# Kernel optimization log

Measured on AMD Instinct MI355X. Metric: run time of the kernel, lower is better.

Reference implementation:

```python
import jax, jax.numpy as jnp
import numpy as np

B, A, L, M, E = 4096, 64, 16, 4, 10
K = (4, 16, 32)
Q = (2, 4, 6)
P = (32, 128, 256)


def setup_inputs() -> dict:
    key = jax.random.key(0)
    ks = iter(jax.random.split(key, 32))
    inp = {}
    inp['x'] = jax.random.normal(next(ks), (B, A, L, M), dtype=jnp.float32)
    inp['y'] = jax.random.uniform(next(ks), (B, E), dtype=jnp.float32)
    inp['w1'] = jax.random.normal(next(ks), (E, K[0], Q[0], A), dtype=jnp.float32) / (K[0] * Q[0])
    inp['w2'] = jax.random.normal(next(ks), (E, K[1], Q[1], A), dtype=jnp.float32) / (K[1] * Q[1])
    inp['w3'] = jax.random.normal(next(ks), (E, K[2], Q[2], A), dtype=jnp.float32) / (K[2] * Q[2])
    inp['coeff1'] = jax.random.normal(next(ks), (P[0],), dtype=jnp.float32)
    inp['coeff2'] = jax.random.normal(next(ks), (P[1],), dtype=jnp.float32)
    inp['coeff3'] = jax.random.normal(next(ks), (P[2],), dtype=jnp.float32)
    ri = lambda n, hi: jax.random.randint(next(ks), (n,), 0, hi, dtype=jnp.int32)
    inp['i1'] = ri(P[0], L); inp['l1'] = ri(P[0], M)
    inp['k1'] = ri(P[0], K[0]); inp['q1'] = ri(P[0], Q[0])
    inp['i2'] = ri(P[1], L); inp['j2'] = ri(P[1], L)
    inp['l2'] = ri(P[1], M); inp['m2'] = ri(P[1], M)
    inp['k2'] = ri(P[1], K[1]); inp['q2'] = ri(P[1], Q[1])
    inp['i3'] = ri(P[2], L); inp['j3'] = ri(P[2], L); inp['f3'] = ri(P[2], L)
    inp['l3'] = ri(P[2], M); inp['m3'] = ri(P[2], M); inp['g3'] = ri(P[2], M)
    inp['k3'] = ri(P[2], K[2]); inp['q3'] = ri(P[2], Q[2])
    return inp


def _forward(x, y, w1, w2, w3, coeff1, coeff2, coeff3,
             i1, l1, k1, q1,
             i2, j2, l2, m2, k2, q2,
             i3, j3, f3, l3, m3, g3, k3, q3):
    # element-mixed weights: [B, K, Q, A]
    wy1 = jnp.einsum('ekqa,be->bkqa', w1, y)
    wy2 = jnp.einsum('ekqa,be->bkqa', w2, y)
    wy3 = jnp.einsum('ekqa,be->bkqa', w3, y)
    # sparse path contraction (equivalent to dense 'ik,lq,ekqa,bail,be->ba' etc.)
    g1 = jnp.transpose(wy1[:, k1, q1, :], (0, 2, 1))          # [B, A, P1]
    t1 = jnp.einsum('bap,p->ba', x[:, :, i1, l1] * g1, coeff1)
    g2 = jnp.transpose(wy2[:, k2, q2, :], (0, 2, 1))          # [B, A, P2]
    t2 = jnp.einsum('bap,p->ba', x[:, :, i2, l2] * x[:, :, j2, m2] * g2, coeff2)
    g3_ = jnp.transpose(wy3[:, k3, q3, :], (0, 2, 1))         # [B, A, P3]
    t3 = jnp.einsum('bap,p->ba',
                    x[:, :, i3, l3] * x[:, :, j3, m3] * x[:, :, f3, g3] * g3_,
                    coeff3)
    return t1 + t2 + t3  # [B, A] (scalar irrep_out -> flattened view)


def reference(x, y, w1, w2, w3, coeff1, coeff2, coeff3,
              i1, l1, k1, q1,
              i2, j2, l2, m2, k2, q2,
              i3, j3, f3, l3, m3, g3, k3, q3):
    return _forward(x, y, w1, w2, w3, coeff1, coeff2, coeff3,
                    i1, l1, k1, q1,
                    i2, j2, l2, m2, k2, q2,
                    i3, j3, f3, l3, m3, g3, k3, q3)
```

## Files before the change

kernel.cpp:

```cpp
#include <hip/hip_runtime.h>
#include <hip/hip_bf16.h>

typedef _Float16 f16x8 __attribute__((ext_vector_type(8)));
typedef _Float16 f16x4 __attribute__((ext_vector_type(4)));
typedef float    f32x4 __attribute__((ext_vector_type(4)));

constexpr int BB  = 4096;
constexpr int AA  = 64;
constexpr int ED  = 10;
constexpr int P1N = 32, P2N = 128, P3N = 256;
constexpr int PT  = 416;
constexpr int NKS = 13;
constexpr int BCH = 64;
constexpr int NCH = 4;

__global__ void build_idx_kernel(
    const int* __restrict__ i1, const int* __restrict__ l1,
    const int* __restrict__ i2, const int* __restrict__ j2,
    const int* __restrict__ l2, const int* __restrict__ m2,
    const int* __restrict__ i3, const int* __restrict__ j3,
    const int* __restrict__ f3, const int* __restrict__ l3,
    const int* __restrict__ m3, const int* __restrict__ g3,
    unsigned* __restrict__ idxs) {
  const int p = threadIdx.x;
  if (p >= PT) return;
  unsigned sa, sb = 64, sc = 64;
  if (p < P1N) {
    sa = i1[p] * 4 + l1[p];
  } else if (p < P1N + P2N) {
    int pp = p - P1N;
    sa = i2[pp] * 4 + l2[pp];
    sb = j2[pp] * 4 + m2[pp];
  } else {
    int pp = p - P1N - P2N;
    sa = i3[pp] * 4 + l3[pp];
    sb = j3[pp] * 4 + m3[pp];
    sc = f3[pp] * 4 + g3[pp];
  }
  idxs[p] = (sa * 8) | ((sb * 8) << 10) | ((sc * 8) << 20);
}

__global__ void build_cwb_kernel(
    const float* __restrict__ w1, const float* __restrict__ w2, const float* __restrict__ w3,
    const float* __restrict__ c1, const float* __restrict__ c2, const float* __restrict__ c3,
    const int* __restrict__ k1, const int* __restrict__ q1,
    const int* __restrict__ k2, const int* __restrict__ q2,
    const int* __restrict__ k3, const int* __restrict__ q3,
    _Float16* __restrict__ cwb) {
  const int a  = blockIdx.x & 63;
  const int ks = blockIdx.x >> 6;
  const int l  = threadIdx.x;
  const int grp = l >> 4, e = l & 15;
  _Float16* dst = cwb + (((size_t)a * NKS + ks) * 64 + l) * 8;
  #pragma unroll
  for (int j = 0; j < 8; ++j) {
    const int p = ks * 32 + grp * 8 + j;
    float v = 0.f;
    if (e < ED) {
      const float* w; float coeff; int k, q, K, Q;
      if (p < P1N)            { w = w1; coeff = c1[p]; k = k1[p]; q = q1[p]; K = 4;  Q = 2; }
      else if (p < P1N + P2N) { int pp = p - P1N;       w = w2; coeff = c2[pp]; k = k2[pp]; q = q2[pp]; K = 16; Q = 4; }
      else                    { int pp = p - P1N - P2N; w = w3; coeff = c3[pp]; k = k3[pp]; q = q3[pp]; K = 32; Q = 6; }
      v = coeff * w[(((size_t)e * K + k) * Q + q) * AA + a];
    }
    dst[j] = (_Float16)v;
  }
}

template <int NF, int KS>
__device__ __forceinline__ void kstep(
    const char* __restrict__ rowb, const uint4* __restrict__ ip,
    const f16x8* __restrict__ cw0, const f16x8* __restrict__ cw1,
    const f16x8* __restrict__ cw2, const f16x8* __restrict__ cw3,
    f32x4& ac0, f32x4& ac1, f32x4& ac2, f32x4& ac3) {
  const uint4 iA = ip[KS * 8 + 0];
  const uint4 iB = ip[KS * 8 + 1];
  const f16x8 b0 = cw0[KS * 64];
  const f16x8 b1 = cw1[KS * 64];
  const f16x8 b2 = cw2[KS * 64];
  const f16x8 b3 = cw3[KS * 64];
  const unsigned pks[8] = {iA.x, iA.y, iA.z, iA.w, iB.x, iB.y, iB.z, iB.w};
  f16x8 af0, af1, af2, af3;
  #pragma unroll
  for (int jh = 0; jh < 2; ++jh) {
    f16x4 g0[4], g1[4], g2[4];
    #pragma unroll
    for (int j = 0; j < 4; ++j) {
      const unsigned pk = pks[jh * 4 + j];
      g0[j] = *(const f16x4*)(rowb + (pk & 1023u));
      if (NF >= 2) g1[j] = *(const f16x4*)(rowb + ((pk >> 10) & 1023u));
      if (NF >= 3) g2[j] = *(const f16x4*)(rowb + (pk >> 20));
    }
    #pragma unroll
    for (int j = 0; j < 4; ++j) {
      f16x4 v = g0[j];
      if (NF >= 2) v = v * g1[j];
      if (NF >= 3) v = v * g2[j];
      const int jj = jh * 4 + j;
      af0[jj] = v[0]; af1[jj] = v[1]; af2[jj] = v[2]; af3[jj] = v[3];
    }
  }
  ac0 = __builtin_amdgcn_mfma_f32_16x16x32_f16(af0, b0, ac0, 0, 0, 0);
  ac1 = __builtin_amdgcn_mfma_f32_16x16x32_f16(af1, b1, ac1, 0, 0, 0);
  ac2 = __builtin_amdgcn_mfma_f32_16x16x32_f16(af2, b2, ac2, 0, 0, 0);
  ac3 = __builtin_amdgcn_mfma_f32_16x16x32_f16(af3, b3, ac3, 0, 0, 0);
}

__global__ __launch_bounds__(256, 4)
void contract_kernel(const float* __restrict__ x, const float* __restrict__ y,
                     const unsigned* __restrict__ idxs,
                     const f16x8* __restrict__ cwb,
                     float* __restrict__ out) {
  __shared__ f16x4 xls[BCH][65];
  __shared__ float yls[BCH][17];

  const int t  = threadIdx.x;
  const int a0 = (blockIdx.x & 15) * NCH;
  const int b0 = (blockIdx.x >> 4) * BCH;
  const int wv = t >> 6, l = t & 63, grp = l >> 4, er = l & 15;
  const int r0 = wv * 16;

  #pragma unroll
  for (int i = 0; i < 4; ++i) {
    const int row = r0 + i * 4 + (l >> 4);
    const int s   = (l & 15) * 4;
    const float* xb = x + (size_t)(b0 + row) * 4096 + a0 * 64 + s;
    const float4 L0 = *(const float4*)(xb);
    const float4 L1 = *(const float4*)(xb + 64);
    const float4 L2 = *(const float4*)(xb + 128);
    const float4 L3 = *(const float4*)(xb + 192);
    f16x4 v0, v1, v2, v3;
    v0[0] = (_Float16)L0.x; v0[1] = (_Float16)L1.x; v0[2] = (_Float16)L2.x; v0[3] = (_Float16)L3.x;
    v1[0] = (_Float16)L0.y; v1[1] = (_Float16)L1.y; v1[2] = (_Float16)L2.y; v1[3] = (_Float16)L3.y;
    v2[0] = (_Float16)L0.z; v2[1] = (_Float16)L1.z; v2[2] = (_Float16)L2.z; v2[3] = (_Float16)L3.z;
    v3[0] = (_Float16)L0.w; v3[1] = (_Float16)L1.w; v3[2] = (_Float16)L2.w; v3[3] = (_Float16)L3.w;
    xls[row][s + 0] = v0;
    xls[row][s + 1] = v1;
    xls[row][s + 2] = v2;
    xls[row][s + 3] = v3;
  }
  if (l < 16) {
    f16x4 one;
    one[0] = one[1] = one[2] = one[3] = (_Float16)1.0f;
    xls[r0 + l][64] = one;
    const float* yb = y + (size_t)(b0 + r0 + l) * ED;
    #pragma unroll
    for (int e = 0; e < ED; ++e) yls[r0 + l][e] = yb[e];
    #pragma unroll
    for (int e = ED; e < 16; ++e) yls[r0 + l][e] = 0.f;
  }

  const char* __restrict__ rowb = (const char*)&xls[r0 + er][0];
  const f16x8* __restrict__ cw0 = cwb + ((size_t)(a0 + 0) * NKS) * 64 + l;
  const f16x8* __restrict__ cw1 = cwb + ((size_t)(a0 + 1) * NKS) * 64 + l;
  const f16x8* __restrict__ cw2 = cwb + ((size_t)(a0 + 2) * NKS) * 64 + l;
  const f16x8* __restrict__ cw3 = cwb + ((size_t)(a0 + 3) * NKS) * 64 + l;
  const uint4*  __restrict__ ip  = (const uint4*)idxs + grp * 2;

  f32x4 a0A = {0.f, 0.f, 0.f, 0.f}, a1A = a0A, a2A = a0A, a3A = a0A;
  f32x4 a0B = a0A, a1B = a0A, a2B = a0A, a3B = a0A;

  #define SA(NF, KS) \
    kstep<NF, KS>(rowb, ip, cw0, cw1, cw2, cw3, a0A, a1A, a2A, a3A)
  #define SB(NF, KS) \
    kstep<NF, KS>(rowb, ip, cw0, cw1, cw2, cw3, a0B, a1B, a2B, a3B)
  SA(1, 0);  SB(3, 7);
  SA(2, 1);  SB(3, 8);
  SA(2, 2);  SB(3, 9);
  SA(2, 3);  SB(3, 10);
  SA(2, 4);  SB(3, 11);
  SA(3, 5);  SB(3, 12);
  SA(3, 6);
  #undef SA
  #undef SB

  const f32x4 ac0 = a0A + a0B;
  const f32x4 ac1 = a1A + a1B;
  const f32x4 ac2 = a2A + a2B;
  const f32x4 ac3 = a3A + a3B;

  #pragma unroll
  for (int c = 0; c < NCH; ++c) {
    const f32x4 acc = c == 0 ? ac0 : c == 1 ? ac1 : c == 2 ? ac2 : ac3;
    float s0 = acc[0] * yls[r0 + grp * 4 + 0][er];
    float s1 = acc[1] * yls[r0 + grp * 4 + 1][er];
    float s2 = acc[2] * yls[r0 + grp * 4 + 2][er];
    float s3 = acc[3] * yls[r0 + grp * 4 + 3][er];
    #pragma unroll
    for (int m = 1; m < 16; m <<= 1) {
      s0 += __shfl_xor(s0, m);
      s1 += __shfl_xor(s1, m);
      s2 += __shfl_xor(s2, m);
      s3 += __shfl_xor(s3, m);
    }
    if (er < 4) {
      const float sv = er == 0 ? s0 : er == 1 ? s1 : er == 2 ? s2 : s3;
      out[(size_t)(b0 + r0 + grp * 4 + er) * AA + (a0 + c)] = sv;
    }
  }
}

extern "C" void kernel_launch(void* const* d_in, const int* in_sizes, int n_in,
                              void* d_out, int out_size, void* d_ws, size_t ws_size,
                              hipStream_t stream) {
  const float* x  = (const float*)d_in[0];
  const float* y  = (const float*)d_in[1];
  const float* w1 = (const float*)d_in[2];
  const float* w2 = (const float*)d_in[3];
  const float* w3 = (const float*)d_in[4];
  const float* c1 = (const float*)d_in[5];
  const float* c2 = (const float*)d_in[6];
  const float* c3 = (const float*)d_in[7];
  const int* i1 = (const int*)d_in[8];
  const int* l1 = (const int*)d_in[9];
  const int* k1 = (const int*)d_in[10];
  const int* q1 = (const int*)d_in[11];
  const int* i2 = (const int*)d_in[12];
  const int* j2 = (const int*)d_in[13];
  const int* l2 = (const int*)d_in[14];
  const int* m2 = (const int*)d_in[15];
  const int* k2 = (const int*)d_in[16];
  const int* q2 = (const int*)d_in[17];
  const int* i3 = (const int*)d_in[18];
  const int* j3 = (const int*)d_in[19];
  const int* f3 = (const int*)d_in[20];
  const int* l3 = (const int*)d_in[21];
  const int* m3 = (const int*)d_in[22];
  const int* g3 = (const int*)d_in[23];
  const int* k3 = (const int*)d_in[24];
  const int* q3 = (const int*)d_in[25];

  unsigned*  idxs = (unsigned*)d_ws;
  _Float16*  cwb  = (_Float16*)((char*)d_ws + 4096);

  build_idx_kernel<<<1, 448, 0, stream>>>(i1, l1, i2, j2, l2, m2,
                                          i3, j3, f3, l3, m3, g3, idxs);
  build_cwb_kernel<<<AA * NKS, 64, 0, stream>>>(w1, w2, w3, c1, c2, c3,
                                                k1, q1, k2, q2, k3, q3, cwb);
  contract_kernel<<<(AA / NCH) * (BB / BCH), 256, 0, stream>>>(
      x, y, idxs, (const f16x8*)cwb, (float*)d_out);
}
```

Baseline: 38.77 us.

## Merge table-building kernels and interleave per-channel weights for contiguous loads

Folds the index-building kernel into the weight-table kernel as one extra block, which saves a kernel launch. The weight table is also relaid so the four output channels for a lane sit next to each other, letting each k-step read the four B operands from one contiguous 64-byte region through a single base pointer. This should cut launch overhead and improve load coalescing and address arithmetic in the main contraction, at the cost of a slightly more complex table layout.

```diff
diff --git a/kernel.cpp b/kernel.cpp
--- a/kernel.cpp
+++ b/kernel.cpp
@@ -14,44 +14,44 @@
 constexpr int BCH = 64;
 constexpr int NCH = 4;
 
-__global__ void build_idx_kernel(
+__global__ void build_tables_kernel(
+    const float* __restrict__ w1, const float* __restrict__ w2, const float* __restrict__ w3,
+    const float* __restrict__ c1, const float* __restrict__ c2, const float* __restrict__ c3,
+    const int* __restrict__ k1, const int* __restrict__ q1,
+    const int* __restrict__ k2, const int* __restrict__ q2,
+    const int* __restrict__ k3, const int* __restrict__ q3,
     const int* __restrict__ i1, const int* __restrict__ l1,
     const int* __restrict__ i2, const int* __restrict__ j2,
     const int* __restrict__ l2, const int* __restrict__ m2,
     const int* __restrict__ i3, const int* __restrict__ j3,
     const int* __restrict__ f3, const int* __restrict__ l3,
     const int* __restrict__ m3, const int* __restrict__ g3,
-    unsigned* __restrict__ idxs) {
-  const int p = threadIdx.x;
-  if (p >= PT) return;
-  unsigned sa, sb = 64, sc = 64;
-  if (p < P1N) {
-    sa = i1[p] * 4 + l1[p];
-  } else if (p < P1N + P2N) {
-    int pp = p - P1N;
-    sa = i2[pp] * 4 + l2[pp];
-    sb = j2[pp] * 4 + m2[pp];
-  } else {
-    int pp = p - P1N - P2N;
-    sa = i3[pp] * 4 + l3[pp];
-    sb = j3[pp] * 4 + m3[pp];
-    sc = f3[pp] * 4 + g3[pp];
-  }
-  idxs[p] = (sa * 8) | ((sb * 8) << 10) | ((sc * 8) << 20);
-}
-
-__global__ void build_cwb_kernel(
-    const float* __restrict__ w1, const float* __restrict__ w2, const float* __restrict__ w3,
-    const float* __restrict__ c1, const float* __restrict__ c2, const float* __restrict__ c3,
-    const int* __restrict__ k1, const int* __restrict__ q1,
-    const int* __restrict__ k2, const int* __restrict__ q2,
-    const int* __restrict__ k3, const int* __restrict__ q3,
-    _Float16* __restrict__ cwb) {
+    _Float16* __restrict__ cwb, unsigned* __restrict__ idxs) {
+  if (blockIdx.x == AA * NKS) {
+    for (int p = threadIdx.x; p < PT; p += 64) {
+      unsigned sa, sb = 64, sc = 64;
+      if (p < P1N) {
+        sa = i1[p] * 4 + l1[p];
+      } else if (p < P1N + P2N) {
+        int pp = p - P1N;
+        sa = i2[pp] * 4 + l2[pp];
+        sb = j2[pp] * 4 + m2[pp];
+      } else {
+        int pp = p - P1N - P2N;
+        sa = i3[pp] * 4 + l3[pp];
+        sb = j3[pp] * 4 + m3[pp];
+        sc = f3[pp] * 4 + g3[pp];
+      }
+      idxs[p] = (sa * 8) | ((sb * 8) << 10) | ((sc * 8) << 20);
+    }
+    return;
+  }
   const int a  = blockIdx.x & 63;
   const int ks = blockIdx.x >> 6;
   const int l  = threadIdx.x;
   const int grp = l >> 4, e = l & 15;
-  _Float16* dst = cwb + (((size_t)a * NKS + ks) * 64 + l) * 8;
+  const int aq = a >> 2, ch = a & 3;
+  _Float16* dst = cwb + ((((size_t)aq * NKS + ks) * 64 + l) * 4 + ch) * 8;
   #pragma unroll
   for (int j = 0; j < 8; ++j) {
     const int p = ks * 32 + grp * 8 + j;
@@ -70,15 +70,15 @@
 template <int NF, int KS>
 __device__ __forceinline__ void kstep(
     const char* __restrict__ rowb, const uint4* __restrict__ ip,
-    const f16x8* __restrict__ cw0, const f16x8* __restrict__ cw1,
-    const f16x8* __restrict__ cw2, const f16x8* __restrict__ cw3,
+    const f16x8* __restrict__ cwq,
     f32x4& ac0, f32x4& ac1, f32x4& ac2, f32x4& ac3) {
   const uint4 iA = ip[KS * 8 + 0];
   const uint4 iB = ip[KS * 8 + 1];
-  const f16x8 b0 = cw0[KS * 64];
-  const f16x8 b1 = cw1[KS * 64];
-  const f16x8 b2 = cw2[KS * 64];
-  const f16x8 b3 = cw3[KS * 64];
+  const f16x8* c = cwq + KS * 256;
+  const f16x8 b0 = c[0];
+  const f16x8 b1 = c[1];
+  const f16x8 b2 = c[2];
+  const f16x8 b3 = c[3];
   const unsigned pks[8] = {iA.x, iA.y, iA.z, iA.w, iB.x, iB.y, iB.z, iB.w};
   f16x8 af0, af1, af2, af3;
   #pragma unroll
@@ -115,7 +115,8 @@
   __shared__ float yls[BCH][17];
 
   const int t  = threadIdx.x;
-  const int a0 = (blockIdx.x & 15) * NCH;
+  const int aq = blockIdx.x & 15;
+  const int a0 = aq * NCH;
   const int b0 = (blockIdx.x >> 4) * BCH;
   const int wv = t >> 6, l = t & 63, grp = l >> 4, er = l & 15;
   const int r0 = wv * 16;
@@ -151,19 +152,14 @@
   }
 
   const char* __restrict__ rowb = (const char*)&xls[r0 + er][0];
-  const f16x8* __restrict__ cw0 = cwb + ((size_t)(a0 + 0) * NKS) * 64 + l;
-  const f16x8* __restrict__ cw1 = cwb + ((size_t)(a0 + 1) * NKS) * 64 + l;
-  const f16x8* __restrict__ cw2 = cwb + ((size_t)(a0 + 2) * NKS) * 64 + l;
-  const f16x8* __restrict__ cw3 = cwb + ((size_t)(a0 + 3) * NKS) * 64 + l;
+  const f16x8* __restrict__ cwq = cwb + (size_t)aq * NKS * 256 + (size_t)l * 4;
   const uint4*  __restrict__ ip  = (const uint4*)idxs + grp * 2;
 
   f32x4 a0A = {0.f, 0.f, 0.f, 0.f}, a1A = a0A, a2A = a0A, a3A = a0A;
   f32x4 a0B = a0A, a1B = a0A, a2B = a0A, a3B = a0A;
 
-  #define SA(NF, KS) \
-    kstep<NF, KS>(rowb, ip, cw0, cw1, cw2, cw3, a0A, a1A, a2A, a3A)
-  #define SB(NF, KS) \
-    kstep<NF, KS>(rowb, ip, cw0, cw1, cw2, cw3, a0B, a1B, a2B, a3B)
+  #define SA(NF, KS) kstep<NF, KS>(rowb, ip, cwq, a0A, a1A, a2A, a3A)
+  #define SB(NF, KS) kstep<NF, KS>(rowb, ip, cwq, a0B, a1B, a2B, a3B)
   SA(1, 0);  SB(3, 7);
   SA(2, 1);  SB(3, 8);
   SA(2, 2);  SB(3, 9);
@@ -233,10 +229,9 @@
   unsigned*  idxs = (unsigned*)d_ws;
   _Float16*  cwb  = (_Float16*)((char*)d_ws + 4096);
 
-  build_idx_kernel<<<1, 448, 0, stream>>>(i1, l1, i2, j2, l2, m2,
-                                          i3, j3, f3, l3, m3, g3, idxs);
-  build_cwb_kernel<<<AA * NKS, 64, 0, stream>>>(w1, w2, w3, c1, c2, c3,
-                                                k1, q1, k2, q2, k3, q3, cwb);
+  build_tables_kernel<<<AA * NKS + 1, 64, 0, stream>>>(
+      w1, w2, w3, c1, c2, c3, k1, q1, k2, q2, k3, q3,
+      i1, l1, i2, j2, l2, m2, i3, j3, f3, l3, m3, g3, cwb, idxs);
   contract_kernel<<<(AA / NCH) * (BB / BCH), 256, 0, stream>>>(
       x, y, idxs, (const f16x8*)cwb, (float*)d_out);
 }
```

Measured after the change: 38.08 us. About the same (-1.8%).
